# Optimization experiments

Measured on AMD Instinct MI355X. Metric: run time of the kernel, lower is better.

The kernel has to match this reference:

```python
import jax, jax.numpy as jnp
import numpy as np

N = 50000
E = 800000
IN_CH = 128
HID = 64
OUT_CH = 40
NUM_LAYERS = 8
ALPHA = 0.1
THETA = 0.5


def setup_inputs() -> dict:
    key = jax.random.key(0)
    ks = jax.random.split(key, 10)
    x = jax.random.normal(ks[0], (N, IN_CH), dtype=jnp.float32)
    edge_src = jax.random.randint(ks[1], (E,), 0, N, dtype=jnp.int32)
    edge_dst = jax.random.randint(ks[2], (E,), 0, N, dtype=jnp.int32)
    edge_weight = jax.random.uniform(ks[3], (E,), dtype=jnp.float32)
    # parameters
    W_in = jax.random.normal(ks[4], (IN_CH, HID), dtype=jnp.float32) / np.sqrt(IN_CH)
    b_in = jnp.zeros((HID,), dtype=jnp.float32)
    W_convs = jax.random.normal(ks[5], (NUM_LAYERS, HID, HID), dtype=jnp.float32) / np.sqrt(HID)
    W_out = jax.random.normal(ks[6], (HID, OUT_CH), dtype=jnp.float32) / np.sqrt(HID)
    b_out = jnp.zeros((OUT_CH,), dtype=jnp.float32)
    return {"x": x, "edge_src": edge_src, "edge_dst": edge_dst,
            "edge_weight": edge_weight, "W_in": W_in, "b_in": b_in,
            "W_convs": W_convs, "W_out": W_out, "b_out": b_out}


def _spmm(edge_src, edge_dst, edge_weight, h):
    # adj_t @ h : gather source features, scale by edge weight, scatter-add to dst
    msg = h[edge_src] * edge_weight[:, None]          # [E, HID]
    return jax.ops.segment_sum(msg, edge_dst, num_segments=N)


def reference(x, edge_src, edge_dst, edge_weight, W_in, b_in, W_convs, W_out, b_out):
    # entry linear + relu (dropout=0 -> identity)
    x0 = jax.nn.relu(x @ W_in + b_in)                 # [N, HID]
    h = x0
    for l in range(NUM_LAYERS):
        beta = float(np.log(THETA / (l + 1) + 1.0))
        agg = _spmm(edge_src, edge_dst, edge_weight, h)
        u = (1.0 - ALPHA) * agg + ALPHA * x0          # initial-residual blend
        out = (1.0 - beta) * u + beta * (u @ W_convs[l])  # identity-mapped weight
        h = jax.nn.relu(out)
    return h @ W_out + b_out                          # [N, OUT_CH]
```

## Files before the change

### kernel.cpp

```cpp
#include <hip/hip_runtime.h>
#include <math.h>

#define NN 50000
#define EE 800000
#define INCH 128
#define HID 64
#define OUTCH 40
#define NUM_LAYERS 8
#define CAP 64

#define EPB 4096
#define NBLK 196
#define NBKT 196

__device__ __forceinline__ float frelu(float v) { return v > 0.f ? v : 0.f; }

__device__ __forceinline__ unsigned int f2bf(float f) {
  unsigned int u = __float_as_uint(f);
  return (u + 0x7fffu + ((u >> 16) & 1u)) >> 16;
}
__device__ __forceinline__ float bf_lo(unsigned int v) { return __uint_as_float(v << 16); }
__device__ __forceinline__ float bf_hi(unsigned int v) { return __uint_as_float(v & 0xffff0000u); }

__global__ __launch_bounds__(256) void entry_gemm(
    const float* __restrict__ x, const float* __restrict__ W,
    const float* __restrict__ b, unsigned int* __restrict__ x0h) {
  __shared__ float Wl[INCH * HID];
  __shared__ float xT[INCH][68];
  __shared__ float bl[HID];
  const int t = threadIdx.x;
  const int base = blockIdx.x * 64;

  #pragma unroll
  for (int i = 0; i < 8; ++i) {
    const int f4 = i * 256 + t;
    *(float4*)&Wl[f4 * 4] = *(const float4*)&W[f4 * 4];
  }
  if (t < HID) bl[t] = b[t];
  #pragma unroll
  for (int i = 0; i < 8; ++i) {
    const int f4 = i * 256 + t;
    const int row = f4 >> 5;
    const int col = (f4 & 31) * 4;
    float4 v = make_float4(0.f, 0.f, 0.f, 0.f);
    if (base + row < NN) v = *(const float4*)&x[(size_t)(base + row) * INCH + col];
    xT[col + 0][row] = v.x; xT[col + 1][row] = v.y;
    xT[col + 2][row] = v.z; xT[col + 3][row] = v.w;
  }
  __syncthreads();

  const int r0 = (t >> 4) * 4;
  const int c0 = (t & 15) * 4;
  float acc[4][4] = {};
  #pragma unroll 4
  for (int k = 0; k < INCH; ++k) {
    const float4 a = *(const float4*)&xT[k][r0];
    const float4 wv = *(const float4*)&Wl[k * HID + c0];
    const float av[4] = {a.x, a.y, a.z, a.w};
    const float wvv[4] = {wv.x, wv.y, wv.z, wv.w};
    #pragma unroll
    for (int i = 0; i < 4; ++i)
      #pragma unroll
      for (int j = 0; j < 4; ++j) acc[i][j] += av[i] * wvv[j];
  }

  #pragma unroll
  for (int i = 0; i < 4; ++i) {
    const int row = base + r0 + i;
    if (row < NN) {
      const float o0 = frelu(acc[i][0] + bl[c0 + 0]);
      const float o1 = frelu(acc[i][1] + bl[c0 + 1]);
      const float o2 = frelu(acc[i][2] + bl[c0 + 2]);
      const float o3 = frelu(acc[i][3] + bl[c0 + 3]);
      uint2 pw;
      pw.x = f2bf(o0) | (f2bf(o1) << 16);
      pw.y = f2bf(o2) | (f2bf(o3) << 16);
      *(uint2*)&x0h[(size_t)row * 32 + (c0 >> 1)] = pw;
    }
  }
}

__global__ __launch_bounds__(256) void edge_hist(const int* __restrict__ dst,
                                                 int* __restrict__ cnt) {
  __shared__ int hist[256];
  const int t = threadIdx.x;
  hist[t] = 0;
  __syncthreads();
  const int e0 = blockIdx.x * EPB;
  #pragma unroll
  for (int i = 0; i < 16; ++i) {
    const int e = e0 + i * 256 + t;
    if (e < EE) atomicAdd(&hist[dst[e] >> 8], 1);
  }
  __syncthreads();
  cnt[t * 200 + blockIdx.x] = hist[t];
}

__global__ __launch_bounds__(256) void scan_cnt(int* __restrict__ cnt,
                                                int* __restrict__ tot) {
  __shared__ int s[2][256];
  const int t = threadIdx.x;
  const int b = blockIdx.x;
  const int v = (t < NBLK) ? cnt[b * 200 + t] : 0;
  int p = 0;
  s[0][t] = v;
  __syncthreads();
  for (int off = 1; off < 256; off <<= 1) {
    s[p ^ 1][t] = s[p][t] + ((t >= off) ? s[p][t - off] : 0);
    p ^= 1;
    __syncthreads();
  }
  if (t < NBLK) cnt[b * 200 + t] = s[p][t] - v;
  if (t == 255) tot[b] = s[p][255];
}

__global__ __launch_bounds__(256) void scan_tot(const int* __restrict__ tot,
                                                int* __restrict__ base) {
  __shared__ int s[2][256];
  const int t = threadIdx.x;
  const int v = (t < NBKT) ? tot[t] : 0;
  int p = 0;
  s[0][t] = v;
  __syncthreads();
  for (int off = 1; off < 256; off <<= 1) {
    s[p ^ 1][t] = s[p][t] + ((t >= off) ? s[p][t - off] : 0);
    p ^= 1;
    __syncthreads();
  }
  base[t] = s[p][t] - v;
}

__global__ __launch_bounds__(256) void edge_place(
    const int* __restrict__ src, const int* __restrict__ dst,
    const float* __restrict__ w, const int* __restrict__ cnt,
    const int* __restrict__ base, uint2* __restrict__ buf8) {
  __shared__ int cur[256];
  const int t = threadIdx.x;
  cur[t] = (t < NBKT) ? (base[t] + cnt[t * 200 + blockIdx.x]) : 0;
  __syncthreads();
  const int e0 = blockIdx.x * EPB;
  #pragma unroll
  for (int i = 0; i < 16; ++i) {
    const int e = e0 + i * 256 + t;
    if (e < EE) {
      const int d = dst[e];
      const int pos = atomicAdd(&cur[d >> 8], 1);
      const unsigned int w15 = (unsigned int)rintf(w[e] * 32767.f);
      buf8[pos] = make_uint2(((unsigned int)src[e] << 15) | w15,
                             (unsigned int)(d & 255));
    }
  }
}

__global__ __launch_bounds__(256) void bucket_place(
    const int* __restrict__ base, const int* __restrict__ tot,
    const uint2* __restrict__ buf8, unsigned int* __restrict__ edges4,
    int* __restrict__ counts) {
  __shared__ int cur2[256];
  const int t = threadIdx.x;
  const int b = blockIdx.x;
  cur2[t] = 0;
  __syncthreads();
  const int start = base[b];
  const int n = tot[b];
  for (int i = t; i < n; i += 256) {
    const uint2 rec = buf8[start + i];
    const int pos = atomicAdd(&cur2[rec.y], 1);
    if (pos < CAP)
      edges4[(size_t)((b << 8) + rec.y) * CAP + pos] = rec.x;
  }
  __syncthreads();
  const int node = (b << 8) + t;
  if (node < NN) counts[node] = min(cur2[t], CAP);
}

__global__ __launch_bounds__(256) void layer_fused(
    const int* __restrict__ counts, const unsigned int* __restrict__ edges4,
    const unsigned int* __restrict__ hin, const unsigned int* __restrict__ x0h,
    const float* __restrict__ W, float beta, unsigned int* __restrict__ hout) {
  __shared__ float Wl[HID * HID];
  __shared__ float uT[32][68];
  const int t = threadIdx.x;
  const int g = t >> 3;
  const int li = t & 7;
  const int gb = (t & 63) & 56;
  const int node = blockIdx.x * 32 + g;
  const float wscale = 1.f / 32767.f;
  const uint4* hrows = (const uint4*)hin;

  #pragma unroll
  for (int i = 0; i < 4; ++i) {
    const int f4 = i * 256 + t;
    *(float4*)&Wl[f4 * 4] = *(const float4*)&W[f4 * 4];
  }

  float a[8] = {0.f, 0.f, 0.f, 0.f, 0.f, 0.f, 0.f, 0.f};
  if (node < NN) {
    const int deg = counts[node];
    const int be = node * CAP;
    for (int e0 = 0; e0 < deg; e0 += 8) {
      const unsigned int ev = edges4[be + e0 + li];
      unsigned int e_[8];
      uint4 h_[8];
      float w_[8];
      #pragma unroll
      for (int m = 0; m < 8; ++m) e_[m] = __shfl(ev, gb + m);
      #pragma unroll
      for (int m = 0; m < 8; ++m) {
        h_[m] = hrows[(size_t)(e_[m] >> 15) * 8 + li];
        w_[m] = (float)(e_[m] & 32767u) * wscale;
      }
      #pragma unroll
      for (int m = 0; m < 8; ++m) {
        a[0] += w_[m] * bf_lo(h_[m].x); a[1] += w_[m] * bf_hi(h_[m].x);
        a[2] += w_[m] * bf_lo(h_[m].y); a[3] += w_[m] * bf_hi(h_[m].y);
        a[4] += w_[m] * bf_lo(h_[m].z); a[5] += w_[m] * bf_hi(h_[m].z);
        a[6] += w_[m] * bf_lo(h_[m].w); a[7] += w_[m] * bf_hi(h_[m].w);
      }
    }
    const uint4 xq = ((const uint4*)x0h)[(size_t)node * 8 + li];
    float4 uA, uB;
    uA.x = 0.9f * a[0] + 0.1f * bf_lo(xq.x);
    uA.y = 0.9f * a[1] + 0.1f * bf_hi(xq.x);
    uA.z = 0.9f * a[2] + 0.1f * bf_lo(xq.y);
    uA.w = 0.9f * a[3] + 0.1f * bf_hi(xq.y);
    uB.x = 0.9f * a[4] + 0.1f * bf_lo(xq.z);
    uB.y = 0.9f * a[5] + 0.1f * bf_hi(xq.z);
    uB.z = 0.9f * a[6] + 0.1f * bf_lo(xq.w);
    uB.w = 0.9f * a[7] + 0.1f * bf_hi(xq.w);
    *(float4*)&uT[g][8 * li + 0] = uA;
    *(float4*)&uT[g][8 * li + 4] = uB;
  }
  __syncthreads();

  const int r0 = (t >> 4) * 2;
  const int c0 = (t & 15) * 4;
  float acc[2][4] = {};
  #pragma unroll 4
  for (int k = 0; k < HID; ++k) {
    const float u0 = uT[r0 + 0][k];
    const float u1 = uT[r0 + 1][k];
    const float4 wq = *(const float4*)&Wl[k * HID + c0];
    acc[0][0] += u0 * wq.x; acc[0][1] += u0 * wq.y;
    acc[0][2] += u0 * wq.z; acc[0][3] += u0 * wq.w;
    acc[1][0] += u1 * wq.x; acc[1][1] += u1 * wq.y;
    acc[1][2] += u1 * wq.z; acc[1][3] += u1 * wq.w;
  }

  const float omb = 1.f - beta;
  #pragma unroll
  for (int i = 0; i < 2; ++i) {
    const int row = blockIdx.x * 32 + r0 + i;
    if (row < NN) {
      const float4 uq = *(const float4*)&uT[r0 + i][c0];
      const float o0 = frelu(omb * uq.x + beta * acc[i][0]);
      const float o1 = frelu(omb * uq.y + beta * acc[i][1]);
      const float o2 = frelu(omb * uq.z + beta * acc[i][2]);
      const float o3 = frelu(omb * uq.w + beta * acc[i][3]);
      uint2 pw;
      pw.x = f2bf(o0) | (f2bf(o1) << 16);
      pw.y = f2bf(o2) | (f2bf(o3) << 16);
      *(uint2*)&hout[(size_t)row * 32 + (c0 >> 1)] = pw;
    }
  }
}

__global__ __launch_bounds__(256) void out_gemm(
    const unsigned int* __restrict__ hp, const float* __restrict__ W,
    const float* __restrict__ b, float* __restrict__ out) {
  __shared__ float hl[64][65];
  __shared__ float Wl[HID * OUTCH];
  __shared__ float bl[OUTCH];
  const int t = threadIdx.x;
  const int base = blockIdx.x * 64;

  #pragma unroll
  for (int i = 0; i < 8; ++i) {
    const int idx = i * 256 + t;
    const int row = idx >> 5;
    const int c = idx & 31;
    unsigned int v = 0;
    if (base + row < NN) v = hp[(size_t)(base + row) * 32 + c];
    hl[row][2 * c + 0] = bf_lo(v);
    hl[row][2 * c + 1] = bf_hi(v);
  }
  for (int i = t; i < HID * OUTCH; i += 256) Wl[i] = W[i];
  if (t < OUTCH) bl[t] = b[t];
  __syncthreads();

  const int r = t & 63;
  const int g = t >> 6;
  const int c0 = g * 10;
  float acc[10] = {};
  for (int k = 0; k < HID; ++k) {
    const float hv = hl[r][k];
    #pragma unroll
    for (int j = 0; j < 10; ++j) acc[j] += hv * Wl[k * OUTCH + c0 + j];
  }
  const int row = base + r;
  if (row < NN) {
    #pragma unroll
    for (int j = 0; j < 10; ++j) out[(size_t)row * OUTCH + c0 + j] = acc[j] + bl[c0 + j];
  }
}

extern "C" void kernel_launch(void* const* d_in, const int* in_sizes, int n_in,
                              void* d_out, int out_size, void* d_ws, size_t ws_size,
                              hipStream_t stream) {
  const float* x     = (const float*)d_in[0];
  const int* esrc    = (const int*)d_in[1];
  const int* edst    = (const int*)d_in[2];
  const float* ew    = (const float*)d_in[3];
  const float* W_in  = (const float*)d_in[4];
  const float* b_in  = (const float*)d_in[5];
  const float* W_cv  = (const float*)d_in[6];
  const float* W_out = (const float*)d_in[7];
  const float* b_out = (const float*)d_in[8];
  float* out = (float*)d_out;

  char* w = (char*)d_ws;
  unsigned int* x0h    = (unsigned int*)(w + 0);
  unsigned int* hA     = (unsigned int*)(w + 6400000);
  unsigned int* hB     = (unsigned int*)(w + 12800000);
  int* counts          = (int*)(w + 19200000);
  int* cnt             = (int*)(w + 19400064);
  int* tot             = (int*)(w + 19604864);
  int* base            = (int*)(w + 19605888);
  uint2* buf8          = (uint2*)(w + 19606912);
  unsigned int* edges4 = (unsigned int*)(w + 26006912);

  const int gemm_grid  = (NN + 63) / 64;
  const int layer_grid = (NN + 31) / 32;

  entry_gemm<<<gemm_grid, 256, 0, stream>>>(x, W_in, b_in, x0h);

  hipMemsetAsync(edges4, 0, (size_t)NN * CAP * sizeof(unsigned int), stream);
  edge_hist<<<NBLK, 256, 0, stream>>>(edst, cnt);
  scan_cnt<<<NBKT, 256, 0, stream>>>(cnt, tot);
  scan_tot<<<1, 256, 0, stream>>>(tot, base);
  edge_place<<<NBLK, 256, 0, stream>>>(esrc, edst, ew, cnt, base, buf8);
  bucket_place<<<NBKT, 256, 0, stream>>>(base, tot, buf8, edges4, counts);

  const unsigned int* hin = x0h;
  unsigned int* hcur = hA;
  for (int l = 0; l < NUM_LAYERS; ++l) {
    const float beta = logf(0.5f / (float)(l + 1) + 1.0f);
    layer_fused<<<layer_grid, 256, 0, stream>>>(counts, edges4, hin, x0h,
                                                W_cv + (size_t)l * HID * HID,
                                                beta, hcur);
    hin = hcur;
    hcur = (hcur == hA) ? hB : hA;
  }

  out_gemm<<<gemm_grid, 256, 0, stream>>>((const unsigned int*)hin, W_out, b_out, out);
}
```

Baseline: 250.7 us.

## Split each node's edge list by source half and pad locally instead of memset

Bucketing now keys on destination block plus whether the source index lies in the lower or upper half of the nodes, giving two edge lists per node with a cap of 40 each. Each layer's gather walks the lower-source list first and then the upper one, which is meant to improve cache locality of the feature-row gathers. The full memset of the edge table is replaced by zero-padding only up to the next multiple of eight per list. This adds more buckets and scan work, plus an extra loop over two halves with possible tail waste in the layer kernel.

```diff
diff --git a/kernel.cpp b/kernel.cpp
--- a/kernel.cpp
+++ b/kernel.cpp
@@ -7,11 +7,12 @@
 #define HID 64
 #define OUTCH 40
 #define NUM_LAYERS 8
-#define CAP 64
 
 #define EPB 4096
 #define NBLK 196
-#define NBKT 196
+#define NBKT2 392
+#define CAP2 40
+#define SRC_SPLIT 25000
 
 __device__ __forceinline__ float frelu(float v) { return v > 0.f ? v : 0.f; }
 
@@ -80,20 +81,27 @@
   }
 }
 
-__global__ __launch_bounds__(256) void edge_hist(const int* __restrict__ dst,
-                                                 int* __restrict__ cnt) {
-  __shared__ int hist[256];
+
+__global__ __launch_bounds__(256) void edge_hist(
+    const int* __restrict__ src, const int* __restrict__ dst,
+    int* __restrict__ cnt) {
+  __shared__ int hist[NBKT2];
   const int t = threadIdx.x;
   hist[t] = 0;
+  if (t + 256 < NBKT2) hist[t + 256] = 0;
   __syncthreads();
   const int e0 = blockIdx.x * EPB;
   #pragma unroll
   for (int i = 0; i < 16; ++i) {
     const int e = e0 + i * 256 + t;
-    if (e < EE) atomicAdd(&hist[dst[e] >> 8], 1);
+    if (e < EE) {
+      const int bkt = ((dst[e] >> 8) << 1) + (src[e] >= SRC_SPLIT);
+      atomicAdd(&hist[bkt], 1);
+    }
   }
   __syncthreads();
   cnt[t * 200 + blockIdx.x] = hist[t];
+  if (t + 256 < NBKT2) cnt[(t + 256) * 200 + blockIdx.x] = hist[t + 256];
 }
 
 __global__ __launch_bounds__(256) void scan_cnt(int* __restrict__ cnt,
@@ -114,29 +122,30 @@
   if (t == 255) tot[b] = s[p][255];
 }
 
-__global__ __launch_bounds__(256) void scan_tot(const int* __restrict__ tot,
+__global__ __launch_bounds__(512) void scan_tot(const int* __restrict__ tot,
                                                 int* __restrict__ base) {
-  __shared__ int s[2][256];
-  const int t = threadIdx.x;
-  const int v = (t < NBKT) ? tot[t] : 0;
+  __shared__ int s[2][512];
+  const int t = threadIdx.x;
+  const int v = (t < NBKT2) ? tot[t] : 0;
   int p = 0;
   s[0][t] = v;
   __syncthreads();
-  for (int off = 1; off < 256; off <<= 1) {
+  for (int off = 1; off < 512; off <<= 1) {
     s[p ^ 1][t] = s[p][t] + ((t >= off) ? s[p][t - off] : 0);
     p ^= 1;
     __syncthreads();
   }
-  base[t] = s[p][t] - v;
+  if (t < NBKT2) base[t] = s[p][t] - v;
 }
 
 __global__ __launch_bounds__(256) void edge_place(
     const int* __restrict__ src, const int* __restrict__ dst,
     const float* __restrict__ w, const int* __restrict__ cnt,
     const int* __restrict__ base, uint2* __restrict__ buf8) {
-  __shared__ int cur[256];
-  const int t = threadIdx.x;
-  cur[t] = (t < NBKT) ? (base[t] + cnt[t * 200 + blockIdx.x]) : 0;
+  __shared__ int cur[NBKT2];
+  const int t = threadIdx.x;
+  if (t < NBKT2) cur[t] = base[t] + cnt[t * 200 + blockIdx.x];
+  if (t + 256 < NBKT2) cur[t + 256] = base[t + 256] + cnt[(t + 256) * 200 + blockIdx.x];
   __syncthreads();
   const int e0 = blockIdx.x * EPB;
   #pragma unroll
@@ -144,9 +153,11 @@
     const int e = e0 + i * 256 + t;
     if (e < EE) {
       const int d = dst[e];
-      const int pos = atomicAdd(&cur[d >> 8], 1);
+      const int s = src[e];
+      const int bkt = ((d >> 8) << 1) + (s >= SRC_SPLIT);
+      const int pos = atomicAdd(&cur[bkt], 1);
       const unsigned int w15 = (unsigned int)rintf(w[e] * 32767.f);
-      buf8[pos] = make_uint2(((unsigned int)src[e] << 15) | w15,
+      buf8[pos] = make_uint2(((unsigned int)s << 15) | w15,
                              (unsigned int)(d & 255));
     }
   }
@@ -155,10 +166,12 @@
 __global__ __launch_bounds__(256) void bucket_place(
     const int* __restrict__ base, const int* __restrict__ tot,
     const uint2* __restrict__ buf8, unsigned int* __restrict__ edges4,
-    int* __restrict__ counts) {
+    int* __restrict__ counts2) {
   __shared__ int cur2[256];
   const int t = threadIdx.x;
   const int b = blockIdx.x;
+  const int half = b & 1;
+  const int nodebase = (b >> 1) << 8;
   cur2[t] = 0;
   __syncthreads();
   const int start = base[b];
@@ -166,16 +179,22 @@
   for (int i = t; i < n; i += 256) {
     const uint2 rec = buf8[start + i];
     const int pos = atomicAdd(&cur2[rec.y], 1);
-    if (pos < CAP)
-      edges4[(size_t)((b << 8) + rec.y) * CAP + pos] = rec.x;
-  }
-  __syncthreads();
-  const int node = (b << 8) + t;
-  if (node < NN) counts[node] = min(cur2[t], CAP);
+    if (pos < CAP2)
+      edges4[(size_t)((nodebase + rec.y) * 2 + half) * CAP2 + pos] = rec.x;
+  }
+  __syncthreads();
+  const int node = nodebase + t;
+  if (node < NN) {
+    const int deg = min(cur2[t], CAP2);
+    const int be = (node * 2 + half) * CAP2;
+    const int pe = min((deg + 7) & ~7, CAP2);
+    for (int i = deg; i < pe; ++i) edges4[be + i] = 0;
+    counts2[node * 2 + half] = deg;
+  }
 }
 
 __global__ __launch_bounds__(256) void layer_fused(
-    const int* __restrict__ counts, const unsigned int* __restrict__ edges4,
+    const int* __restrict__ counts2, const unsigned int* __restrict__ edges4,
     const unsigned int* __restrict__ hin, const unsigned int* __restrict__ x0h,
     const float* __restrict__ W, float beta, unsigned int* __restrict__ hout) {
   __shared__ float Wl[HID * HID];
@@ -196,26 +215,29 @@
 
   float a[8] = {0.f, 0.f, 0.f, 0.f, 0.f, 0.f, 0.f, 0.f};
   if (node < NN) {
-    const int deg = counts[node];
-    const int be = node * CAP;
-    for (int e0 = 0; e0 < deg; e0 += 8) {
-      const unsigned int ev = edges4[be + e0 + li];
-      unsigned int e_[8];
-      uint4 h_[8];
-      float w_[8];
-      #pragma unroll
-      for (int m = 0; m < 8; ++m) e_[m] = __shfl(ev, gb + m);
-      #pragma unroll
-      for (int m = 0; m < 8; ++m) {
-        h_[m] = hrows[(size_t)(e_[m] >> 15) * 8 + li];
-        w_[m] = (float)(e_[m] & 32767u) * wscale;
-      }
-      #pragma unroll
-      for (int m = 0; m < 8; ++m) {
-        a[0] += w_[m] * bf_lo(h_[m].x); a[1] += w_[m] * bf_hi(h_[m].x);
-        a[2] += w_[m] * bf_lo(h_[m].y); a[3] += w_[m] * bf_hi(h_[m].y);
-        a[4] += w_[m] * bf_lo(h_[m].z); a[5] += w_[m] * bf_hi(h_[m].z);
-        a[6] += w_[m] * bf_lo(h_[m].w); a[7] += w_[m] * bf_hi(h_[m].w);
+    #pragma unroll
+    for (int half = 0; half < 2; ++half) {
+      const int deg = counts2[node * 2 + half];
+      const int be = (node * 2 + half) * CAP2;
+      for (int e0 = 0; e0 < deg; e0 += 8) {
+        const unsigned int ev = edges4[be + e0 + li];
+        unsigned int e_[8];
+        uint4 h_[8];
+        float w_[8];
+        #pragma unroll
+        for (int m = 0; m < 8; ++m) e_[m] = __shfl(ev, gb + m);
+        #pragma unroll
+        for (int m = 0; m < 8; ++m) {
+          h_[m] = hrows[(size_t)(e_[m] >> 15) * 8 + li];
+          w_[m] = (float)(e_[m] & 32767u) * wscale;
+        }
+        #pragma unroll
+        for (int m = 0; m < 8; ++m) {
+          a[0] += w_[m] * bf_lo(h_[m].x); a[1] += w_[m] * bf_hi(h_[m].x);
+          a[2] += w_[m] * bf_lo(h_[m].y); a[3] += w_[m] * bf_hi(h_[m].y);
+          a[4] += w_[m] * bf_lo(h_[m].z); a[5] += w_[m] * bf_hi(h_[m].z);
+          a[6] += w_[m] * bf_lo(h_[m].w); a[7] += w_[m] * bf_hi(h_[m].w);
+        }
       }
     }
     const uint4 xq = ((const uint4*)x0h)[(size_t)node * 8 + li];
@@ -322,30 +344,29 @@
   unsigned int* x0h    = (unsigned int*)(w + 0);
   unsigned int* hA     = (unsigned int*)(w + 6400000);
   unsigned int* hB     = (unsigned int*)(w + 12800000);
-  int* counts          = (int*)(w + 19200000);
-  int* cnt             = (int*)(w + 19400064);
-  int* tot             = (int*)(w + 19604864);
-  int* base            = (int*)(w + 19605888);
-  uint2* buf8          = (uint2*)(w + 19606912);
-  unsigned int* edges4 = (unsigned int*)(w + 26006912);
+  int* counts2         = (int*)(w + 19200000);
+  int* cnt             = (int*)(w + 19600000);
+  int* tot             = (int*)(w + 19913600);
+  int* base            = (int*)(w + 19915648);
+  uint2* buf8          = (uint2*)(w + 19917696);
+  unsigned int* edges4 = (unsigned int*)(w + 26317696);
 
   const int gemm_grid  = (NN + 63) / 64;
   const int layer_grid = (NN + 31) / 32;
 
   entry_gemm<<<gemm_grid, 256, 0, stream>>>(x, W_in, b_in, x0h);
 
-  hipMemsetAsync(edges4, 0, (size_t)NN * CAP * sizeof(unsigned int), stream);
-  edge_hist<<<NBLK, 256, 0, stream>>>(edst, cnt);
-  scan_cnt<<<NBKT, 256, 0, stream>>>(cnt, tot);
-  scan_tot<<<1, 256, 0, stream>>>(tot, base);
+  edge_hist<<<NBLK, 256, 0, stream>>>(esrc, edst, cnt);
+  scan_cnt<<<NBKT2, 256, 0, stream>>>(cnt, tot);
+  scan_tot<<<1, 512, 0, stream>>>(tot, base);
   edge_place<<<NBLK, 256, 0, stream>>>(esrc, edst, ew, cnt, base, buf8);
-  bucket_place<<<NBKT, 256, 0, stream>>>(base, tot, buf8, edges4, counts);
+  bucket_place<<<NBKT2, 256, 0, stream>>>(base, tot, buf8, edges4, counts2);
 
   const unsigned int* hin = x0h;
   unsigned int* hcur = hA;
   for (int l = 0; l < NUM_LAYERS; ++l) {
     const float beta = logf(0.5f / (float)(l + 1) + 1.0f);
-    layer_fused<<<layer_grid, 256, 0, stream>>>(counts, edges4, hin, x0h,
+    layer_fused<<<layer_grid, 256, 0, stream>>>(counts2, edges4, hin, x0h,
                                                 W_cv + (size_t)l * HID * HID,
                                                 beta, hcur);
     hin = hcur;
```

Measured after the change: 259.9 us. 1.04x slower.
